# Performance work log

Hardware: AMD Instinct MI355X
Metric: run time of the kernel (lower is better)

Reference implementation:

```python
import jax, jax.numpy as jnp
import numpy as np

B, L, D, H, OUT = 4, 2048, 1024, 8, 256
DH = D // H
EPS = 1e-12


def setup_inputs() -> dict:
    key = jax.random.key(0)
    ks = jax.random.split(key, 20)
    s = lambda fan_in: 1.0 / np.sqrt(fan_in)
    def lin(k, fin, fout):
        k1, k2 = jax.random.split(k)
        w = jax.random.uniform(k1, (fin, fout), jnp.float32, -s(fin), s(fin))
        b = jax.random.uniform(k2, (fout,), jnp.float32, -s(fin), s(fin))
        return w, b
    x = jax.random.normal(ks[0], (B, L, D), jnp.float32)
    wq, bq = lin(ks[1], D, D)
    wk, bk = lin(ks[2], D, D)
    wv, bv = lin(ks[3], D, D)
    gamma = jnp.ones((D,), jnp.float32)
    beta = jnp.zeros((D,), jnp.float32)
    wff, bff = lin(ks[4], D, D)
    wc1, bc1 = lin(ks[5], D, D)
    wc2, bc2 = lin(ks[6], D, 1)
    wl1, bl1 = lin(ks[7], L, L)
    wl2, bl2 = lin(ks[8], L, OUT)
    return dict(x=x, wq=wq, bq=bq, wk=wk, bk=bk, wv=wv, bv=bv,
                gamma=gamma, beta=beta, wff=wff, bff=bff,
                wc1=wc1, bc1=bc1, wc2=wc2, bc2=bc2,
                wl1=wl1, bl1=bl1, wl2=wl2, bl2=bl2)


def layernorm(x, gamma, beta):
    mean = x.mean(-1, keepdims=True)
    var = ((x - mean) ** 2).mean(-1, keepdims=True)  # biased variance
    return gamma * (x - mean) / jnp.sqrt(var + EPS) + beta


def reference(x, wq, bq, wk, bk, wv, bv, gamma, beta, wff, bff,
              wc1, bc1, wc2, bc2, wl1, bl1, wl2, bl2):
    # multi-head self-attention (dropout = identity at inference)
    q = (x @ wq + bq).reshape(B, L, H, DH)
    k = (x @ wk + bk).reshape(B, L, H, DH)
    v = (x @ wv + bv).reshape(B, L, H, DH)
    scores = jnp.einsum('bqhd,bkhd->bhqk', q, k) / np.sqrt(DH)
    attn = jax.nn.softmax(scores, axis=-1)                  # [B,H,L,L]
    ctx = jnp.einsum('bhqk,bkhd->bqhd', attn, v).reshape(B, L, D)
    h = layernorm(x + ctx, gamma, beta)
    # feedforward: Linear + ReLU (hidden = d_model), residual + same layernorm params
    ff = jax.nn.relu(h @ wff + bff)
    h = layernorm(h + ff, gamma, beta)
    # collapse d_model -> 1
    c = jax.nn.relu(h @ wc1 + bc1)
    c = jax.nn.relu(c @ wc2 + bc2)                          # [B,L,1]
    c = jnp.squeeze(c, axis=-1)                             # [B,L]
    # collapse length -> out_featuresize
    c = jax.nn.relu(c @ wl1 + bl1)
    out = c @ wl2 + bl2                                     # [B,OUT]
    return out
```

## Files before the change

kernel.cpp:

```cpp
#include <hip/hip_runtime.h>

typedef unsigned short u16;
typedef unsigned int u32;
typedef __attribute__((ext_vector_type(4))) float f32x4;
typedef __attribute__((ext_vector_type(8))) short short8;
typedef __attribute__((ext_vector_type(4))) u32 u32x4;
typedef __attribute__((ext_vector_type(4))) u16 u16x4;

#define BB 4
#define LL 2048
#define DD 1024
#define HH 8
#define DHH 128

__device__ __forceinline__ u16 f2b(float f) {
  u32 u = __builtin_bit_cast(u32, f);
  u += 0x7fffu + ((u >> 16) & 1u);
  return (u16)(u >> 16);
}
__device__ __forceinline__ float b2f(u16 h) {
  u32 u = ((u32)h) << 16;
  return __builtin_bit_cast(float, u);
}
__device__ __forceinline__ float exp2_fast(float x) {
  float r;
  asm("v_exp_f32 %0, %1" : "=v"(r) : "v"(x));
  return r;
}
__device__ __forceinline__ u32 packbf(float a, float b) {
  return (u32)f2b(a) | ((u32)f2b(b) << 16);
}
__device__ __forceinline__ u32 bperm(int srcLane, u32 v) {
  return (u32)__builtin_amdgcn_ds_bpermute(srcLane << 2, (int)v);
}

#define GLDS16(g, l)                                                          \
  __builtin_amdgcn_global_load_lds(                                           \
      (const __attribute__((address_space(1))) void*)(g),                     \
      (__attribute__((address_space(3))) void*)(l), 16, 0, 0)

__global__ __launch_bounds__(256) void cvt_k(const float* __restrict__ X,
                                             u16* __restrict__ Xb, long n) {
  long i = ((long)blockIdx.x * 256 + threadIdx.x) * 4;
  if (i >= n) return;
  f32x4 v = *(const f32x4*)(X + i);
  u16x4 o;
#pragma unroll
  for (int k = 0; k < 4; k++) o[k] = f2b(v[k]);
  *(u16x4*)(Xb + i) = o;
}

__global__ __launch_bounds__(256) void tr_k(const float* __restrict__ W,
                                            u16* __restrict__ WT) {
  __shared__ float tile[32][33];
  const int bx = blockIdx.x, by = blockIdx.y;
  const int tx = threadIdx.x & 31, ty = threadIdx.x >> 5;
#pragma unroll
  for (int i = 0; i < 4; i++)
    tile[ty + i * 8][tx] =
        W[(long)(by * 32 + ty + i * 8) * 1024 + bx * 32 + tx];
  __syncthreads();
#pragma unroll
  for (int i = 0; i < 4; i++)
    WT[(long)(bx * 32 + ty + i * 8) * 1024 + by * 32 + tx] =
        f2b(tile[tx][ty + i * 8]);
}

__global__ __launch_bounds__(256, 4) void qkv_k(
    const u16* __restrict__ A, const u16* __restrict__ QT,
    const u16* __restrict__ KT, const u16* __restrict__ VTw,
    const float* __restrict__ bq, const float* __restrict__ bk,
    const float* __restrict__ bv, float qscale, u16* __restrict__ Qo,
    u16* __restrict__ Ko, u16* __restrict__ Vo) {
  __shared__ u16 As[2][128 * 32];
  __shared__ u16 Bs[2][128 * 32];
  const int K = 1024;
  const int nwg = gridDim.x * gridDim.y;
  const int bid = blockIdx.x + blockIdx.y * gridDim.x;
  const int swz = (bid & 7) * (nwg >> 3) + (bid >> 3);
  const int bxi = swz % 24, byi = swz / 24;
  const int sector = bxi >> 3;
  const u16* BT = sector == 0 ? QT : (sector == 1 ? KT : VTw);
  const float* bias = sector == 0 ? bq : (sector == 1 ? bk : bv);
  const float scale = sector == 0 ? qscale : 1.f;
  const int t = threadIdx.x;
  const int l = t & 63, w = t >> 6;
  const int lr = l & 15, lg = l >> 4;
  const int wr = (w >> 1) * 64, wc = (w & 1) * 64;
  const long bm = (long)byi * 128, bn = (long)(bxi & 7) * 128;
  const int srow = l >> 2;
  const int scol = (l & 3) * 8;
  const u16* Ag0 = A + (bm + w * 32 + srow) * (long)K + scol;
  const u16* Ag1 = A + (bm + w * 32 + 16 + srow) * (long)K + scol;
  const u16* Bg0 = BT + (bn + w * 32 + srow) * (long)K + scol;
  const u16* Bg1 = BT + (bn + w * 32 + 16 + srow) * (long)K + scol;
  const int wo = w * 1024;
  f32x4 acc[4][4] = {};
  GLDS16(Ag0, &As[0][wo]);
  GLDS16(Ag1, &As[0][wo + 512]);
  GLDS16(Bg0, &Bs[0][wo]);
  GLDS16(Bg1, &Bs[0][wo + 512]);
  __syncthreads();
  int cur = 0;
  for (int k0 = 0; k0 < K; k0 += 32) {
    const int nxt = cur ^ 1;
    if (k0 + 32 < K) {
      GLDS16(Ag0 + k0 + 32, &As[nxt][wo]);
      GLDS16(Ag1 + k0 + 32, &As[nxt][wo + 512]);
      GLDS16(Bg0 + k0 + 32, &Bs[nxt][wo]);
      GLDS16(Bg1 + k0 + 32, &Bs[nxt][wo + 512]);
    }
    short8 af[4], bf[4];
#pragma unroll
    for (int i = 0; i < 4; i++)
      af[i] = *(const short8*)&As[cur][(wr + i * 16 + lr) * 32 + lg * 8];
#pragma unroll
    for (int i = 0; i < 4; i++)
      bf[i] = *(const short8*)&Bs[cur][(wc + i * 16 + lr) * 32 + lg * 8];
#pragma unroll
    for (int i = 0; i < 4; i++)
#pragma unroll
      for (int j = 0; j < 4; j++)
        acc[i][j] = __builtin_amdgcn_mfma_f32_16x16x32_bf16(af[i], bf[j],
                                                            acc[i][j], 0, 0, 0);
    __syncthreads();
    cur = nxt;
  }
#pragma unroll
  for (int i = 0; i < 4; i++)
#pragma unroll
    for (int j = 0; j < 4; j++) {
      long col = bn + wc + j * 16 + lr;
      float bvv = bias[col];
      if (sector == 2) {
        long row0 = bm + wr + i * 16 + lg * 4;
        long b = row0 >> 11, l0 = row0 & 2047;
        u16x4 ov;
#pragma unroll
        for (int r = 0; r < 4; r++) ov[r] = f2b(acc[i][j][r] + bvv);
        *(u16x4*)(Vo + (b * 1024 + col) * 2048 + l0) = ov;
      } else {
        u16* Out = sector == 0 ? Qo : Ko;
#pragma unroll
        for (int r = 0; r < 4; r++) {
          long row = bm + wr + i * 16 + lg * 4 + r;
          Out[row * 1024 + col] = f2b((acc[i][j][r] + bvv) * scale);
        }
      }
    }
}

template <bool RELU, int OMODE>
__global__ __launch_bounds__(256, 3) void gemm_k(
    const u16* __restrict__ A, const u16* __restrict__ BT,
    const float* __restrict__ bias, float scale, float* __restrict__ Cf,
    u16* __restrict__ Cb, const float* __restrict__ w2,
    float* __restrict__ cvec, int M, int N, int K) {
  __shared__ u16 As[2][128 * 32];
  __shared__ u16 Bs[2][128 * 32];
  const int nwg = gridDim.x * gridDim.y;
  const int bid = blockIdx.x + blockIdx.y * gridDim.x;
  const int swz = (bid & 7) * (nwg >> 3) + (bid >> 3);
  const int bxi = swz % gridDim.x, byi = swz / gridDim.x;
  const int t = threadIdx.x;
  const int l = t & 63, w = t >> 6;
  const int lr = l & 15, lg = l >> 4;
  const int wr = (w >> 1) * 64, wc = (w & 1) * 64;
  const long bm = (long)byi * 128, bn = (long)bxi * 128;
  const int srow = l >> 2;
  const int scol = (l & 3) * 8;
  const u16* Ag0 = A + (bm + w * 32 + srow) * (long)K + scol;
  const u16* Ag1 = A + (bm + w * 32 + 16 + srow) * (long)K + scol;
  const u16* Bg0 = BT + (bn + w * 32 + srow) * (long)K + scol;
  const u16* Bg1 = BT + (bn + w * 32 + 16 + srow) * (long)K + scol;
  const int wo = w * 1024;
  f32x4 acc[4][4] = {};
  GLDS16(Ag0, &As[0][wo]);
  GLDS16(Ag1, &As[0][wo + 512]);
  GLDS16(Bg0, &Bs[0][wo]);
  GLDS16(Bg1, &Bs[0][wo + 512]);
  __syncthreads();
  int cur = 0;
  for (int k0 = 0; k0 < K; k0 += 32) {
    const int nxt = cur ^ 1;
    if (k0 + 32 < K) {
      GLDS16(Ag0 + k0 + 32, &As[nxt][wo]);
      GLDS16(Ag1 + k0 + 32, &As[nxt][wo + 512]);
      GLDS16(Bg0 + k0 + 32, &Bs[nxt][wo]);
      GLDS16(Bg1 + k0 + 32, &Bs[nxt][wo + 512]);
    }
    short8 af[4], bf[4];
#pragma unroll
    for (int i = 0; i < 4; i++)
      af[i] = *(const short8*)&As[cur][(wr + i * 16 + lr) * 32 + lg * 8];
#pragma unroll
    for (int i = 0; i < 4; i++)
      bf[i] = *(const short8*)&Bs[cur][(wc + i * 16 + lr) * 32 + lg * 8];
#pragma unroll
    for (int i = 0; i < 4; i++)
#pragma unroll
      for (int j = 0; j < 4; j++)
        acc[i][j] = __builtin_amdgcn_mfma_f32_16x16x32_bf16(af[i], bf[j],
                                                            acc[i][j], 0, 0, 0);
    __syncthreads();
    cur = nxt;
  }
  if (OMODE == 3) {
    float bvj[4], w2j[4];
#pragma unroll
    for (int j = 0; j < 4; j++) {
      long col = bn + wc + j * 16 + lr;
      bvj[j] = bias[col];
      w2j[j] = w2[col];
    }
#pragma unroll
    for (int i = 0; i < 4; i++)
#pragma unroll
      for (int r = 0; r < 4; r++) {
        float a2 = 0.f;
#pragma unroll
        for (int j = 0; j < 4; j++)
          a2 += fmaxf(acc[i][j][r] + bvj[j], 0.f) * w2j[j];
        a2 += __shfl_xor(a2, 1, 64);
        a2 += __shfl_xor(a2, 2, 64);
        a2 += __shfl_xor(a2, 4, 64);
        a2 += __shfl_xor(a2, 8, 64);
        if (lr == 0) {
          long row = bm + wr + i * 16 + lg * 4 + r;
          atomicAdd(&cvec[row], a2);
        }
      }
  } else {
#pragma unroll
    for (int i = 0; i < 4; i++)
#pragma unroll
      for (int j = 0; j < 4; j++) {
        long col = bn + wc + j * 16 + lr;
        float bv = bias[col];
#pragma unroll
        for (int r = 0; r < 4; r++) {
          long row = bm + wr + i * 16 + lg * 4 + r;
          float v2 = (acc[i][j][r] + bv) * scale;
          if (RELU) v2 = fmaxf(v2, 0.f);
          Cf[row * N + col] = v2;
        }
      }
  }
}

__global__ __launch_bounds__(512, 4) void flash_k(const u16* __restrict__ Q,
                                                  const u16* __restrict__ Kb,
                                                  const u16* __restrict__ VT,
                                                  float* __restrict__ ctx) {
  __shared__ u16 Ks2[2][64 * 128];
  __shared__ u16 Vs2[2][128 * 64];
  const int nwg = gridDim.x * gridDim.y;
  const int bid = blockIdx.x + blockIdx.y * gridDim.x;
  const int swz = (bid & 7) * (nwg >> 3) + (bid >> 3);
  const int bxi = swz % gridDim.x, byi = swz / gridDim.x;
  const int t = threadIdx.x;
  const int l = t & 63, w = t >> 6;
  const int lr = l & 15, lg = l >> 4;
  const int b = byi >> 3, h = byi & 7;
  const long kbase = ((long)b * LL) * DD + h * DHH;
  const long vtbase = ((long)(b * 8 + h) * DHH) * LL;
  const int q0 = bxi * 128;

  short8 qf[4];
  {
    const u16* qp = Q + kbase + (long)(q0 + w * 16 + lr) * DD + lg * 8;
#pragma unroll
    for (int c = 0; c < 4; c++) qf[c] = *(const short8*)(qp + c * 32);
  }
  f32x4 oacc[8] = {};
  float mprev = -1e30f;
  float lsum = 0.f;

  const int krA = w * 8 + (l >> 4);
  const int krB = krA + 4;
  const int kc16 = l & 15;
  const int vrA = w * 16 + (l >> 3);
  const int vrB = vrA + 8;
  const int vc16 = l & 7;
  const u16* kg0 = Kb + kbase + (long)krA * DD + (kc16 ^ (krA & 7)) * 8;
  const u16* kg1 = Kb + kbase + (long)krB * DD + (kc16 ^ (krB & 7)) * 8;
  const u16* vg0 = VT + vtbase + (long)vrA * LL + (vc16 ^ (vrA & 7)) * 8;
  const u16* vg1 = VT + vtbase + (long)vrB * LL + (vc16 ^ (vrB & 7)) * 8;
  u16* const kl0 = &Ks2[0][(w * 8) * 128];
  u16* const kl1 = &Ks2[0][(w * 8 + 4) * 128];
  u16* const vl0 = &Vs2[0][(w * 16) * 64];
  u16* const vl1 = &Vs2[0][(w * 16 + 8) * 64];
  GLDS16(kg0, kl0);
  GLDS16(kg1, kl1);
  GLDS16(vg0, vl0);
  GLDS16(vg1, vl1);
  __syncthreads();

  int colk[4], colv[2];
#pragma unroll
  for (int c = 0; c < 4; c++) colk[c] = (((c * 4 + lg) ^ (lr & 7)) * 8);
#pragma unroll
  for (int kk = 0; kk < 2; kk++) colv[kk] = (((kk * 4 + lg) ^ (lr & 7)) * 8);

  const int NT = LL / 64;
  for (int it = 0; it < NT; ++it) {
    const int cur = it & 1;
    if (it + 1 < NT) {
      kg0 += 64 * DD;
      kg1 += 64 * DD;
      vg0 += 64;
      vg1 += 64;
      const int ko = (cur ^ 1) * (64 * 128);
      const int vo = (cur ^ 1) * (128 * 64);
      GLDS16(kg0, kl0 + ko);
      GLDS16(kg1, kl1 + ko);
      GLDS16(vg0, vl0 + vo);
      GLDS16(vg1, vl1 + vo);
    }
    const u16* Kc = &Ks2[cur][0];
    const u16* Vc = &Vs2[cur][0];

    f32x4 s[4] = {};
#pragma unroll
    for (int jc = 0; jc < 4; jc++)
#pragma unroll
      for (int c = 0; c < 4; c++) {
        short8 kf = *(const short8*)&Kc[(jc * 16 + lr) * 128 + colk[c]];
        s[jc] =
            __builtin_amdgcn_mfma_f32_16x16x32_bf16(kf, qf[c], s[jc], 0, 0, 0);
      }

    float mx = fmaxf(fmaxf(s[0][0], s[0][1]), fmaxf(s[0][2], s[0][3]));
#pragma unroll
    for (int jc = 1; jc < 4; jc++)
      mx = fmaxf(mx, fmaxf(fmaxf(s[jc][0], s[jc][1]),
                           fmaxf(s[jc][2], s[jc][3])));
    mx = fmaxf(mx, __shfl_xor(mx, 16, 64));
    mx = fmaxf(mx, __shfl_xor(mx, 32, 64));

    if (__any((int)(mx > mprev + 8.f))) {
      float mn = fmaxf(mprev, mx);
      float alpha = exp2_fast(mprev - mn);
      mprev = mn;
      lsum *= alpha;
      float ar[4];
#pragma unroll
      for (int r = 0; r < 4; r++) ar[r] = __shfl(alpha, lg * 4 + r, 64);
#pragma unroll
      for (int d8 = 0; d8 < 8; d8++)
#pragma unroll
        for (int r = 0; r < 4; r++) oacc[d8][r] *= ar[r];
    }

    u32 pk2[4][2];
    float ladd = 0.f;
#pragma unroll
    for (int jc = 0; jc < 4; jc++) {
      float p0 = exp2_fast(s[jc][0] - mprev);
      float p1 = exp2_fast(s[jc][1] - mprev);
      float p2 = exp2_fast(s[jc][2] - mprev);
      float p3 = exp2_fast(s[jc][3] - mprev);
      ladd += (p0 + p1) + (p2 + p3);
      pk2[jc][0] = packbf(p0, p1);
      pk2[jc][1] = packbf(p2, p3);
    }
    lsum += ladd;

    short8 pf[2];
#pragma unroll
    for (int kk = 0; kk < 2; kk++) {
      u32x4 afv;
#pragma unroll
      for (int m = 0; m < 4; m++) {
        int srcl = lr + ((((lg & 1) << 1) + (m >> 1)) << 4);
        u32 a0 = bperm(srcl, pk2[2 * kk][m & 1]);
        u32 a1 = bperm(srcl, pk2[2 * kk + 1][m & 1]);
        afv[m] = (lg >> 1) ? a1 : a0;
      }
      pf[kk] = __builtin_bit_cast(short8, afv);
    }

#pragma unroll
    for (int kk = 0; kk < 2; kk++)
#pragma unroll
      for (int d8 = 0; d8 < 8; d8++) {
        short8 vf = *(const short8*)&Vc[(d8 * 16 + lr) * 64 + colv[kk]];
        oacc[d8] =
            __builtin_amdgcn_mfma_f32_16x16x32_bf16(pf[kk], vf, oacc[d8], 0,
                                                    0, 0);
      }
    __syncthreads();
  }

  lsum += __shfl_xor(lsum, 16, 64);
  lsum += __shfl_xor(lsum, 32, 64);
#pragma unroll
  for (int r = 0; r < 4; r++) {
    float inv = 1.f / __shfl(lsum, lg * 4 + r, 64);
    float* cp = ctx + kbase + (long)(q0 + w * 16 + lg * 4 + r) * DD;
#pragma unroll
    for (int d8 = 0; d8 < 8; d8++) cp[d8 * 16 + lr] = oacc[d8][r] * inv;
  }
}

__global__ __launch_bounds__(256) void ln_k(const float* __restrict__ X,
                                            const float* __restrict__ R,
                                            const float* __restrict__ gamma,
                                            const float* __restrict__ beta,
                                            float* __restrict__ Hf,
                                            u16* __restrict__ Hb) {
  const int row = blockIdx.x, t = threadIdx.x;
  const long off = (long)row * DD + t * 4;
  f32x4 v = *(const f32x4*)(X + off);
  f32x4 rv = *(const f32x4*)(R + off);
#pragma unroll
  for (int i = 0; i < 4; i++) v[i] += rv[i];
  float s = v[0] + v[1] + v[2] + v[3];
  float q = v[0] * v[0] + v[1] * v[1] + v[2] * v[2] + v[3] * v[3];
#pragma unroll
  for (int m = 32; m >= 1; m >>= 1) {
    s += __shfl_xor(s, m, 64);
    q += __shfl_xor(q, m, 64);
  }
  __shared__ float red[8];
  if ((t & 63) == 0) {
    red[t >> 6] = s;
    red[4 + (t >> 6)] = q;
  }
  __syncthreads();
  s = red[0] + red[1] + red[2] + red[3];
  q = red[4] + red[5] + red[6] + red[7];
  const float mean = s * (1.f / 1024.f);
  const float var = q * (1.f / 1024.f) - mean * mean;
  const float rstd = rsqrtf(var + 1e-12f);
  f32x4 g = *(const f32x4*)(gamma + t * 4);
  f32x4 be = *(const f32x4*)(beta + t * 4);
  f32x4 o;
#pragma unroll
  for (int i = 0; i < 4; i++) o[i] = g[i] * (v[i] - mean) * rstd + be[i];
  if (Hf) *(f32x4*)(Hf + off) = o;
  if (Hb) {
    u16x4 ob;
#pragma unroll
    for (int i = 0; i < 4; i++) ob[i] = f2b(o[i]);
    *(u16x4*)(Hb + off) = ob;
  }
}

template <bool BR>
__global__ __launch_bounds__(256) void smm_part(const float* __restrict__ Cin,
                                                const float* __restrict__ W,
                                                float* __restrict__ P, int Lr,
                                                int N, int SL,
                                                const float* __restrict__ b0) {
  const int j = blockIdx.x * 256 + threadIdx.x;
  const int l0 = blockIdx.y * SL;
  const float bb = BR ? b0[0] : 0.f;
  float a0 = 0, a1 = 0, a2 = 0, a3 = 0;
  for (int ll = l0; ll < l0 + SL; ll++) {
    float wv = W[(long)ll * N + j];
    float c0 = Cin[ll], c1 = Cin[Lr + ll], c2 = Cin[2 * Lr + ll],
          c3 = Cin[3 * Lr + ll];
    if (BR) {
      c0 = fmaxf(c0 + bb, 0.f);
      c1 = fmaxf(c1 + bb, 0.f);
      c2 = fmaxf(c2 + bb, 0.f);
      c3 = fmaxf(c3 + bb, 0.f);
    }
    a0 += c0 * wv;
    a1 += c1 * wv;
    a2 += c2 * wv;
    a3 += c3 * wv;
  }
  float* Pp = P + ((long)blockIdx.y * 4) * N + j;
  Pp[0] = a0;
  Pp[N] = a1;
  Pp[2 * N] = a2;
  Pp[3 * N] = a3;
}

template <bool RELU>
__global__ __launch_bounds__(256) void smm_red(const float* __restrict__ P,
                                               const float* __restrict__ bias,
                                               float* __restrict__ Out, int N,
                                               int S) {
  const int j = blockIdx.x * 256 + threadIdx.x;
#pragma unroll
  for (int b = 0; b < 4; b++) {
    float a = 0;
    for (int s = 0; s < S; s++) a += P[((long)s * 4 + b) * N + j];
    a += bias[j];
    if (RELU) a = fmaxf(a, 0.f);
    Out[(long)b * N + j] = a;
  }
}

extern "C" void kernel_launch(void* const* d_in, const int* in_sizes, int n_in,
                              void* d_out, int out_size, void* d_ws,
                              size_t ws_size, hipStream_t stream) {
  (void)in_sizes; (void)n_in; (void)out_size; (void)ws_size;
  const float* x = (const float*)d_in[0];
  const float* wq = (const float*)d_in[1];
  const float* bq = (const float*)d_in[2];
  const float* wk = (const float*)d_in[3];
  const float* bk = (const float*)d_in[4];
  const float* wv = (const float*)d_in[5];
  const float* bv = (const float*)d_in[6];
  const float* gamma = (const float*)d_in[7];
  const float* beta = (const float*)d_in[8];
  const float* wff = (const float*)d_in[9];
  const float* bff = (const float*)d_in[10];
  const float* wc1 = (const float*)d_in[11];
  const float* bc1 = (const float*)d_in[12];
  const float* wc2 = (const float*)d_in[13];
  const float* bc2 = (const float*)d_in[14];
  const float* wl1 = (const float*)d_in[15];
  const float* bl1 = (const float*)d_in[16];
  const float* wl2 = (const float*)d_in[17];
  const float* bl2 = (const float*)d_in[18];

  char* wsp = (char*)d_ws;
  size_t off = 0;
  auto take = [&](size_t bytes) -> char* {
    char* p = wsp + off;
    off += (bytes + 255) & ~(size_t)255;
    return p;
  };
  u16* xb = (u16*)take((size_t)8192 * 1024 * 2);
  u16* wqT = (u16*)take((size_t)1024 * 1024 * 2);
  u16* wkT = (u16*)take((size_t)1024 * 1024 * 2);
  u16* wvT = (u16*)take((size_t)1024 * 1024 * 2);
  u16* wffT = (u16*)take((size_t)1024 * 1024 * 2);
  u16* wc1T = (u16*)take((size_t)1024 * 1024 * 2);
  u16* qb = (u16*)take((size_t)8192 * 1024 * 2);
  u16* kbuf = (u16*)take((size_t)8192 * 1024 * 2);
  u16* vT = (u16*)take((size_t)8192 * 1024 * 2);
  float* ctxb = (float*)take((size_t)8192 * 1024 * 4);
  float* h1f = (float*)take((size_t)8192 * 1024 * 4);
  float* cvec = (float*)take(8192 * 4);
  float* c3 = (float*)take(8192 * 4);
  float* P1 = (float*)take((size_t)16 * 4 * 2048 * 4);
  float* P2 = (float*)take((size_t)16 * 4 * 256 * 4);
  u16* h1b = qb;
  u16* h2b = kbuf;
  float* ff = ctxb;

  cvt_k<<<8192, 256, 0, stream>>>(x, xb, (long)8192 * 1024);
  dim3 trg(32, 32);
  tr_k<<<trg, 256, 0, stream>>>(wq, wqT);
  tr_k<<<trg, 256, 0, stream>>>(wk, wkT);
  tr_k<<<trg, 256, 0, stream>>>(wv, wvT);
  tr_k<<<trg, 256, 0, stream>>>(wff, wffT);
  tr_k<<<trg, 256, 0, stream>>>(wc1, wc1T);

  qkv_k<<<dim3(24, 64), 256, 0, stream>>>(xb, wqT, wkT, wvT, bq, bk, bv,
                                          0.12751743f, qb, kbuf, vT);
  flash_k<<<dim3(16, 32), 512, 0, stream>>>(qb, kbuf, vT, ctxb);
  ln_k<<<8192, 256, 0, stream>>>(x, ctxb, gamma, beta, h1f, h1b);
  dim3 gg(8, 64);
  gemm_k<true, 0><<<gg, 256, 0, stream>>>(h1b, wffT, bff, 1.f, ff, nullptr,
                                          nullptr, nullptr, 8192, 1024, 1024);
  ln_k<<<8192, 256, 0, stream>>>(h1f, ff, gamma, beta, nullptr, h2b);
  hipMemsetAsync(cvec, 0, 8192 * sizeof(float), stream);
  gemm_k<true, 3><<<gg, 256, 0, stream>>>(h2b, wc1T, bc1, 1.f, nullptr,
                                          nullptr, wc2, cvec, 8192, 1024,
                                          1024);
  smm_part<true><<<dim3(8, 16), 256, 0, stream>>>(cvec, wl1, P1, 2048, 2048,
                                                  128, bc2);
  smm_red<true><<<8, 256, 0, stream>>>(P1, bl1, c3, 2048, 16);
  smm_part<false><<<dim3(1, 16), 256, 0, stream>>>(c3, wl2, P2, 2048, 256,
                                                   128, nullptr);
  smm_red<false><<<1, 256, 0, stream>>>(P2, bl2, (float*)d_out, 256, 16);
}
```

Before: 381.2 us.

## Process two query sub-tiles per wave in flash attention with 4-wave blocks

The flash attention kernel now uses 256 threads (4 waves) per block, each wave handling 32 query rows as two 16-row sub-tiles. Each K and V fragment read from LDS is reused for two MFMAs, halving LDS reads per MFMA, and each thread issues four global-to-LDS copies per tile instead of two. Register pressure roughly doubles (two accumulator sets, two softmax states), so launch bounds drop to 2 blocks/CU, and qkv_k's bound goes from 4 to 3. The risk is lower occupancy and possible spills in exchange for better data reuse.

```diff
diff --git a/kernel.cpp b/kernel.cpp
--- a/kernel.cpp
+++ b/kernel.cpp
@@ -66,7 +66,7 @@
         f2b(tile[tx][ty + i * 8]);
 }
 
-__global__ __launch_bounds__(256, 4) void qkv_k(
+__global__ __launch_bounds__(256, 3) void qkv_k(
     const u16* __restrict__ A, const u16* __restrict__ QT,
     const u16* __restrict__ KT, const u16* __restrict__ VTw,
     const float* __restrict__ bq, const float* __restrict__ bk,
@@ -248,7 +248,7 @@
   }
 }
 
-__global__ __launch_bounds__(512, 4) void flash_k(const u16* __restrict__ Q,
+__global__ __launch_bounds__(256, 2) void flash_k(const u16* __restrict__ Q,
                                                   const u16* __restrict__ Kb,
                                                   const u16* __restrict__ VT,
                                                   float* __restrict__ ctx) {
@@ -266,34 +266,38 @@
   const long vtbase = ((long)(b * 8 + h) * DHH) * LL;
   const int q0 = bxi * 128;
 
-  short8 qf[4];
+  short8 qf0[4], qf1[4];
   {
-    const u16* qp = Q + kbase + (long)(q0 + w * 16 + lr) * DD + lg * 8;
-#pragma unroll
-    for (int c = 0; c < 4; c++) qf[c] = *(const short8*)(qp + c * 32);
-  }
-  f32x4 oacc[8] = {};
-  float mprev = -1e30f;
-  float lsum = 0.f;
-
-  const int krA = w * 8 + (l >> 4);
-  const int krB = krA + 4;
-  const int kc16 = l & 15;
-  const int vrA = w * 16 + (l >> 3);
-  const int vrB = vrA + 8;
-  const int vc16 = l & 7;
-  const u16* kg0 = Kb + kbase + (long)krA * DD + (kc16 ^ (krA & 7)) * 8;
-  const u16* kg1 = Kb + kbase + (long)krB * DD + (kc16 ^ (krB & 7)) * 8;
-  const u16* vg0 = VT + vtbase + (long)vrA * LL + (vc16 ^ (vrA & 7)) * 8;
-  const u16* vg1 = VT + vtbase + (long)vrB * LL + (vc16 ^ (vrB & 7)) * 8;
-  u16* const kl0 = &Ks2[0][(w * 8) * 128];
-  u16* const kl1 = &Ks2[0][(w * 8 + 4) * 128];
-  u16* const vl0 = &Vs2[0][(w * 16) * 64];
-  u16* const vl1 = &Vs2[0][(w * 16 + 8) * 64];
-  GLDS16(kg0, kl0);
-  GLDS16(kg1, kl1);
-  GLDS16(vg0, vl0);
-  GLDS16(vg1, vl1);
+    const u16* qp0 = Q + kbase + (long)(q0 + w * 32 + lr) * DD + lg * 8;
+    const u16* qp1 = qp0 + 16 * DD;
+#pragma unroll
+    for (int c = 0; c < 4; c++) {
+      qf0[c] = *(const short8*)(qp0 + c * 32);
+      qf1[c] = *(const short8*)(qp1 + c * 32);
+    }
+  }
+  f32x4 oacc0[8] = {}, oacc1[8] = {};
+  float mprev0 = -1e30f, mprev1 = -1e30f;
+  float lsum0 = 0.f, lsum1 = 0.f;
+
+  const u16* kg[4];
+  const u16* vg[4];
+  u16* kl[4];
+  u16* vl[4];
+#pragma unroll
+  for (int i = 0; i < 4; i++) {
+    int rk = w * 16 + 4 * i + (l >> 4);
+    kg[i] = Kb + kbase + (long)rk * DD + ((l & 15) ^ (rk & 7)) * 8;
+    kl[i] = &Ks2[0][(w * 16 + 4 * i) * 128];
+    int rv = w * 32 + 8 * i + (l >> 3);
+    vg[i] = VT + vtbase + (long)rv * LL + ((l & 7) ^ (rv & 7)) * 8;
+    vl[i] = &Vs2[0][(w * 32 + 8 * i) * 64];
+  }
+#pragma unroll
+  for (int i = 0; i < 4; i++) {
+    GLDS16(kg[i], kl[i]);
+    GLDS16(vg[i], vl[i]);
+  }
   __syncthreads();
 
   int colk[4], colv[2];
@@ -306,78 +310,105 @@
   for (int it = 0; it < NT; ++it) {
     const int cur = it & 1;
     if (it + 1 < NT) {
-      kg0 += 64 * DD;
-      kg1 += 64 * DD;
-      vg0 += 64;
-      vg1 += 64;
       const int ko = (cur ^ 1) * (64 * 128);
       const int vo = (cur ^ 1) * (128 * 64);
-      GLDS16(kg0, kl0 + ko);
-      GLDS16(kg1, kl1 + ko);
-      GLDS16(vg0, vl0 + vo);
-      GLDS16(vg1, vl1 + vo);
+#pragma unroll
+      for (int i = 0; i < 4; i++) {
+        kg[i] += 64 * DD;
+        vg[i] += 64;
+        GLDS16(kg[i], kl[i] + ko);
+        GLDS16(vg[i], vl[i] + vo);
+      }
     }
     const u16* Kc = &Ks2[cur][0];
     const u16* Vc = &Vs2[cur][0];
 
-    f32x4 s[4] = {};
+    f32x4 s0[4] = {}, s1[4] = {};
 #pragma unroll
     for (int jc = 0; jc < 4; jc++)
 #pragma unroll
       for (int c = 0; c < 4; c++) {
         short8 kf = *(const short8*)&Kc[(jc * 16 + lr) * 128 + colk[c]];
-        s[jc] =
-            __builtin_amdgcn_mfma_f32_16x16x32_bf16(kf, qf[c], s[jc], 0, 0, 0);
-      }
-
-    float mx = fmaxf(fmaxf(s[0][0], s[0][1]), fmaxf(s[0][2], s[0][3]));
-#pragma unroll
-    for (int jc = 1; jc < 4; jc++)
-      mx = fmaxf(mx, fmaxf(fmaxf(s[jc][0], s[jc][1]),
-                           fmaxf(s[jc][2], s[jc][3])));
-    mx = fmaxf(mx, __shfl_xor(mx, 16, 64));
-    mx = fmaxf(mx, __shfl_xor(mx, 32, 64));
-
-    if (__any((int)(mx > mprev + 8.f))) {
-      float mn = fmaxf(mprev, mx);
-      float alpha = exp2_fast(mprev - mn);
-      mprev = mn;
-      lsum *= alpha;
-      float ar[4];
-#pragma unroll
-      for (int r = 0; r < 4; r++) ar[r] = __shfl(alpha, lg * 4 + r, 64);
+        s0[jc] =
+            __builtin_amdgcn_mfma_f32_16x16x32_bf16(kf, qf0[c], s0[jc], 0, 0, 0);
+        s1[jc] =
+            __builtin_amdgcn_mfma_f32_16x16x32_bf16(kf, qf1[c], s1[jc], 0, 0, 0);
+      }
+
+    float mx0 = fmaxf(fmaxf(s0[0][0], s0[0][1]), fmaxf(s0[0][2], s0[0][3]));
+    float mx1 = fmaxf(fmaxf(s1[0][0], s1[0][1]), fmaxf(s1[0][2], s1[0][3]));
+#pragma unroll
+    for (int jc = 1; jc < 4; jc++) {
+      mx0 = fmaxf(mx0, fmaxf(fmaxf(s0[jc][0], s0[jc][1]),
+                             fmaxf(s0[jc][2], s0[jc][3])));
+      mx1 = fmaxf(mx1, fmaxf(fmaxf(s1[jc][0], s1[jc][1]),
+                             fmaxf(s1[jc][2], s1[jc][3])));
+    }
+    mx0 = fmaxf(mx0, __shfl_xor(mx0, 16, 64));
+    mx0 = fmaxf(mx0, __shfl_xor(mx0, 32, 64));
+    mx1 = fmaxf(mx1, __shfl_xor(mx1, 16, 64));
+    mx1 = fmaxf(mx1, __shfl_xor(mx1, 32, 64));
+
+    if (__any((int)((mx0 > mprev0 + 8.f) || (mx1 > mprev1 + 8.f)))) {
+      float mn0 = fmaxf(mprev0, mx0), mn1 = fmaxf(mprev1, mx1);
+      float al0 = exp2_fast(mprev0 - mn0), al1 = exp2_fast(mprev1 - mn1);
+      mprev0 = mn0;
+      mprev1 = mn1;
+      lsum0 *= al0;
+      lsum1 *= al1;
+      float ar0[4], ar1[4];
+#pragma unroll
+      for (int r = 0; r < 4; r++) {
+        ar0[r] = __shfl(al0, lg * 4 + r, 64);
+        ar1[r] = __shfl(al1, lg * 4 + r, 64);
+      }
 #pragma unroll
       for (int d8 = 0; d8 < 8; d8++)
 #pragma unroll
-        for (int r = 0; r < 4; r++) oacc[d8][r] *= ar[r];
-    }
-
-    u32 pk2[4][2];
-    float ladd = 0.f;
+        for (int r = 0; r < 4; r++) {
+          oacc0[d8][r] *= ar0[r];
+          oacc1[d8][r] *= ar1[r];
+        }
+    }
+
+    u32 pk0[4][2], pk1[4][2];
+    float la0 = 0.f, la1 = 0.f;
 #pragma unroll
     for (int jc = 0; jc < 4; jc++) {
-      float p0 = exp2_fast(s[jc][0] - mprev);
-      float p1 = exp2_fast(s[jc][1] - mprev);
-      float p2 = exp2_fast(s[jc][2] - mprev);
-      float p3 = exp2_fast(s[jc][3] - mprev);
-      ladd += (p0 + p1) + (p2 + p3);
-      pk2[jc][0] = packbf(p0, p1);
-      pk2[jc][1] = packbf(p2, p3);
-    }
-    lsum += ladd;
-
-    short8 pf[2];
+      float a0 = exp2_fast(s0[jc][0] - mprev0);
+      float a1 = exp2_fast(s0[jc][1] - mprev0);
+      float a2 = exp2_fast(s0[jc][2] - mprev0);
+      float a3 = exp2_fast(s0[jc][3] - mprev0);
+      la0 += (a0 + a1) + (a2 + a3);
+      pk0[jc][0] = packbf(a0, a1);
+      pk0[jc][1] = packbf(a2, a3);
+      float b0 = exp2_fast(s1[jc][0] - mprev1);
+      float b1 = exp2_fast(s1[jc][1] - mprev1);
+      float b2 = exp2_fast(s1[jc][2] - mprev1);
+      float b3 = exp2_fast(s1[jc][3] - mprev1);
+      la1 += (b0 + b1) + (b2 + b3);
+      pk1[jc][0] = packbf(b0, b1);
+      pk1[jc][1] = packbf(b2, b3);
+    }
+    lsum0 += la0;
+    lsum1 += la1;
+
+    short8 pf0[2], pf1[2];
 #pragma unroll
     for (int kk = 0; kk < 2; kk++) {
-      u32x4 afv;
+      u32x4 av0, av1;
 #pragma unroll
       for (int m = 0; m < 4; m++) {
         int srcl = lr + ((((lg & 1) << 1) + (m >> 1)) << 4);
-        u32 a0 = bperm(srcl, pk2[2 * kk][m & 1]);
-        u32 a1 = bperm(srcl, pk2[2 * kk + 1][m & 1]);
-        afv[m] = (lg >> 1) ? a1 : a0;
-      }
-      pf[kk] = __builtin_bit_cast(short8, afv);
+        u32 x0 = bperm(srcl, pk0[2 * kk][m & 1]);
+        u32 x1 = bperm(srcl, pk0[2 * kk + 1][m & 1]);
+        av0[m] = (lg >> 1) ? x1 : x0;
+        u32 y0 = bperm(srcl, pk1[2 * kk][m & 1]);
+        u32 y1 = bperm(srcl, pk1[2 * kk + 1][m & 1]);
+        av1[m] = (lg >> 1) ? y1 : y0;
+      }
+      pf0[kk] = __builtin_bit_cast(short8, av0);
+      pf1[kk] = __builtin_bit_cast(short8, av1);
     }
 
 #pragma unroll
@@ -385,21 +416,29 @@
 #pragma unroll
       for (int d8 = 0; d8 < 8; d8++) {
         short8 vf = *(const short8*)&Vc[(d8 * 16 + lr) * 64 + colv[kk]];
-        oacc[d8] =
-            __builtin_amdgcn_mfma_f32_16x16x32_bf16(pf[kk], vf, oacc[d8], 0,
-                                                    0, 0);
+        oacc0[d8] = __builtin_amdgcn_mfma_f32_16x16x32_bf16(pf0[kk], vf,
+                                                            oacc0[d8], 0, 0, 0);
+        oacc1[d8] = __builtin_amdgcn_mfma_f32_16x16x32_bf16(pf1[kk], vf,
+                                                            oacc1[d8], 0, 0, 0);
       }
     __syncthreads();
   }
 
-  lsum += __shfl_xor(lsum, 16, 64);
-  lsum += __shfl_xor(lsum, 32, 64);
+  lsum0 += __shfl_xor(lsum0, 16, 64);
+  lsum0 += __shfl_xor(lsum0, 32, 64);
+  lsum1 += __shfl_xor(lsum1, 16, 64);
+  lsum1 += __shfl_xor(lsum1, 32, 64);
 #pragma unroll
   for (int r = 0; r < 4; r++) {
-    float inv = 1.f / __shfl(lsum, lg * 4 + r, 64);
-    float* cp = ctx + kbase + (long)(q0 + w * 16 + lg * 4 + r) * DD;
-#pragma unroll
-    for (int d8 = 0; d8 < 8; d8++) cp[d8 * 16 + lr] = oacc[d8][r] * inv;
+    float inv0 = 1.f / __shfl(lsum0, lg * 4 + r, 64);
+    float inv1 = 1.f / __shfl(lsum1, lg * 4 + r, 64);
+    float* cp0 = ctx + kbase + (long)(q0 + w * 32 + lg * 4 + r) * DD;
+    float* cp1 = cp0 + 16 * DD;
+#pragma unroll
+    for (int d8 = 0; d8 < 8; d8++) {
+      cp0[d8 * 16 + lr] = oacc0[d8][r] * inv0;
+      cp1[d8 * 16 + lr] = oacc1[d8][r] * inv1;
+    }
   }
 }
 
@@ -555,7 +594,7 @@
 
   qkv_k<<<dim3(24, 64), 256, 0, stream>>>(xb, wqT, wkT, wvT, bq, bk, bv,
                                           0.12751743f, qb, kbuf, vT);
-  flash_k<<<dim3(16, 32), 512, 0, stream>>>(qb, kbuf, vT, ctxb);
+  flash_k<<<dim3(16, 32), 256, 0, stream>>>(qb, kbuf, vT, ctxb);
   ln_k<<<8192, 256, 0, stream>>>(x, ctxb, gamma, beta, h1f, h1b);
   dim3 gg(8, 64);
   gemm_k<true, 0><<<gg, 256, 0, stream>>>(h1b, wffT, bff, 1.f, ff, nullptr,
```

After: 378.0 us. Within noise of the previous version (-0.8%).
